# Optimization experiments

Hardware: AMD Instinct MI355X
Metric: run time of the kernel (lower is better)

Reference implementation:

```python
import math
import jax, jax.numpy as jnp
import numpy as np

B, S, D, H = 2, 1024, 4096, 32
HD = D // H  # 128


def _rope_freqs(seq_len, head_dim, theta=10000.0):
    inv = 1.0 / (theta ** (np.arange(0, head_dim, 2, dtype=np.float32) / head_dim))
    t = np.arange(seq_len, dtype=np.float32)
    ang = np.outer(t, inv)  # [S, HD/2]
    return jnp.asarray(np.cos(ang)), jnp.asarray(np.sin(ang))


def setup_inputs() -> dict:
    key = jax.random.key(0)
    ks = jax.random.split(key, 6)
    scale = 0.02
    x = jax.random.normal(ks[0], (B, S, D), dtype=jnp.float32)
    wq = jax.random.normal(ks[1], (D, D), dtype=jnp.float32) * scale
    wk = jax.random.normal(ks[2], (D, D), dtype=jnp.float32) * scale
    wv = jax.random.normal(ks[3], (D, D), dtype=jnp.float32) * scale
    wo = jax.random.normal(ks[4], (D, D), dtype=jnp.float32) * scale
    cache_k = jnp.zeros((B, S, H, HD), dtype=jnp.float32)
    cache_v = jnp.zeros((B, S, H, HD), dtype=jnp.float32)
    freqs_cos, freqs_sin = _rope_freqs(S, HD)
    return {"x": x, "wq": wq, "wk": wk, "wv": wv, "wo": wo,
            "cache_k": cache_k, "cache_v": cache_v,
            "freqs_cos": freqs_cos, "freqs_sin": freqs_sin, "start_pos": 0}


def _apply_rope(t, cos, sin):
    # t: [B, S, H, HD]; pairs (even, odd) along last dim form complex numbers
    t2 = t.reshape(*t.shape[:-1], HD // 2, 2)
    t0, t1 = t2[..., 0], t2[..., 1]
    c = cos[None, :, None, :]  # [1, S, 1, HD/2]
    s = sin[None, :, None, :]
    o0 = t0 * c - t1 * s
    o1 = t0 * s + t1 * c
    return jnp.stack([o0, o1], axis=-1).reshape(t.shape)


def reference(x, wq, wk, wv, wo, cache_k, cache_v, freqs_cos, freqs_sin, start_pos):
    b, s, d = x.shape
    q = (x @ wq.T).reshape(b, s, H, HD)
    k = (x @ wk.T).reshape(b, s, H, HD)  # n_kv_heads == n_heads (n_rep=1)
    v = (x @ wv.T).reshape(b, s, H, HD)
    q = _apply_rope(q, freqs_cos, freqs_sin)
    k = _apply_rope(k, freqs_cos, freqs_sin)
    # KV-cache write, then read the [0 : start_pos+s] window
    cache_k = cache_k.at[:b, start_pos:start_pos + s].set(k)
    cache_v = cache_v.at[:b, start_pos:start_pos + s].set(v)
    keys = cache_k[:b, :start_pos + s]    # [b, T, H, HD]
    values = cache_v[:b, :start_pos + s]
    scores = jnp.einsum("bqhd,bkhd->bhqk", q, keys) / math.sqrt(HD)
    attn = jax.nn.softmax(scores.astype(jnp.float32), axis=-1).astype(q.dtype)
    out = jnp.einsum("bhqk,bkhd->bqhd", attn, values).reshape(b, s, d)
    return out @ wo.T
```

## Files before the change

kernel.cpp:

```cpp
#include <hip/hip_runtime.h>

#define B_  2
#define S_  1024
#define D_  4096
#define H_  32
#define HD_ 128
#define T_  (B_*S_)

typedef short s16x8 __attribute__((ext_vector_type(8)));
typedef float f32x4 __attribute__((ext_vector_type(4)));
typedef unsigned short u16;

__device__ __forceinline__ u16 f2bf(float f) {
  unsigned int u = __float_as_uint(f);
  u += 0x7fffu + ((u >> 16) & 1u);
  return (u16)(u >> 16);
}
__device__ __forceinline__ float bf2f(u16 h) {
  return __uint_as_float(((unsigned int)h) << 16);
}
__device__ __forceinline__ void gload_lds16(const void* g, void* l) {
  __builtin_amdgcn_global_load_lds(
      (const __attribute__((address_space(1))) unsigned int*)g,
      (__attribute__((address_space(3))) unsigned int*)l, 16, 0, 0);
}
#define MFMA16(a, b, c) __builtin_amdgcn_mfma_f32_16x16x32_bf16((a), (b), (c), 0, 0, 0)

__global__ __launch_bounds__(256) void cvt_all(const float* __restrict__ x,
                                               const float* __restrict__ wq,
                                               const float* __restrict__ wk,
                                               const float* __restrict__ wv,
                                               const float* __restrict__ wo,
                                               u16* __restrict__ xb,
                                               u16* __restrict__ wb) {
  const int n8x = T_ * D_ / 8;
  const int n8w = D_ * D_ / 8;
  const int total = n8x + 4 * n8w;
  for (int i = blockIdx.x * 256 + threadIdx.x; i < total; i += gridDim.x * 256) {
    const float* src;
    u16* dst;
    int off;
    if (i < n8x) { src = x; dst = xb; off = i; }
    else {
      const int j = i - n8x;
      const int seg = j >> 21;
      off = j & (n8w - 1);
      src = (seg == 0) ? wq : (seg == 1) ? wk : (seg == 2) ? wv : wo;
      dst = wb + ((size_t)seg << 24);
    }
    const float4* p = (const float4*)src + (size_t)off * 2;
    float4 a = p[0], b = p[1];
    u16 us[8] = {f2bf(a.x), f2bf(a.y), f2bf(a.z), f2bf(a.w),
                 f2bf(b.x), f2bf(b.y), f2bf(b.z), f2bf(b.w)};
    *(uint4*)(dst + (size_t)off * 8) = *(uint4*)us;
  }
}

template <int NW>
__device__ __forceinline__ void stage_tile(const u16* __restrict__ g, int ldk,
                                           int row0, int k0, u16* lds,
                                           int wid, int lane) {
  const int rsub = lane >> 3;
  const int c16  = (lane & 7) ^ rsub;
#pragma unroll
  for (int l = 0; l < 16 / NW; ++l) {
    const int c = wid * (16 / NW) + l;
    gload_lds16(g + (size_t)(row0 + c * 8 + rsub) * ldk + k0 + c16 * 8,
                lds + c * 512);
  }
}

__global__ __launch_bounds__(256, 3) void gemm_qkv(const u16* __restrict__ A,
                                                   const u16* __restrict__ W,
                                                   u16* __restrict__ Oq,
                                                   u16* __restrict__ Ok,
                                                   u16* __restrict__ Ovt,
                                                   const float* __restrict__ cosb,
                                                   const float* __restrict__ sinb,
                                                   int MB, int NB, int K) {
  __shared__ __align__(16) u16 LA[128 * 64];
  __shared__ __align__(16) u16 LB[128 * 64];
  const int nwg = MB * NB;
  const int cpx = nwg >> 3;
  const int bid = blockIdx.x;
  const int swz = (bid & 7) * cpx + (bid >> 3);
  const int bm = swz / NB, bn = swz % NB;
  const int m0 = bm * 128, n0 = bn * 128;
  const int tid = threadIdx.x, wid = tid >> 6, lane = tid & 63;
  const int wr = wid >> 1, wc = wid & 1;
  const int fr = lane & 15, fq = lane >> 4;
  f32x4 acc[4][4] = {};

  for (int k0 = 0; k0 < K; k0 += 64) {
    stage_tile<4>(A, K, m0, k0, LA, wid, lane);
    stage_tile<4>(W, K, n0, k0, LB, wid, lane);
    __syncthreads();
    s16x8 bf[4][2];
#pragma unroll
    for (int ni = 0; ni < 4; ++ni)
#pragma unroll
      for (int kk = 0; kk < 2; ++kk) {
        const int rr = wc * 64 + ni * 16 + fr;
        const int s16 = (kk * 4 + fq) ^ (rr & 7);
        bf[ni][kk] = *(const s16x8*)&LB[rr * 64 + s16 * 8];
      }
#pragma unroll
    for (int mi = 0; mi < 4; ++mi) {
      const int r = wr * 64 + mi * 16 + fr;
      const s16x8 a0 = *(const s16x8*)&LA[r * 64 + ((0 + fq) ^ (r & 7)) * 8];
      const s16x8 a1 = *(const s16x8*)&LA[r * 64 + ((4 + fq) ^ (r & 7)) * 8];
#pragma unroll
      for (int ni = 0; ni < 4; ++ni)
        acc[mi][ni] = MFMA16(a0, bf[ni][0], acc[mi][ni]);
#pragma unroll
      for (int ni = 0; ni < 4; ++ni)
        acc[mi][ni] = MFMA16(a1, bf[ni][1], acc[mi][ni]);
    }
    __syncthreads();
  }

  if (n0 < 8192) {
    u16* Ob = (n0 < 4096) ? Oq : Ok;
    const int nc = n0 & 4095;
    const float sgn = (fr & 1) ? 1.f : -1.f;
#pragma unroll
    for (int mi = 0; mi < 4; ++mi)
#pragma unroll
      for (int ni = 0; ni < 4; ++ni) {
        const int col = nc + wc * 64 + ni * 16 + fr;
        const int i0 = (col & (HD_ - 1)) >> 1;
#pragma unroll
        for (int r = 0; r < 4; ++r) {
          const int row = m0 + wr * 64 + mi * 16 + fq * 4 + r;
          const int s = row & (S_ - 1);
          const float v  = acc[mi][ni][r];
          const float vo = __shfl_xor(v, 1);
          const float c  = cosb[s * (HD_ / 2) + i0];
          const float sn = sinb[s * (HD_ / 2) + i0];
          Ob[(size_t)row * 4096 + col] = f2bf(v * c + sgn * vo * sn);
        }
      }
  } else {
    const int nc = n0 - 8192;
#pragma unroll
    for (int mi = 0; mi < 4; ++mi)
#pragma unroll
      for (int ni = 0; ni < 4; ++ni) {
        const int col = nc + wc * 64 + ni * 16 + fr;
        const int h = col >> 7, d = col & (HD_ - 1);
        const int row0 = m0 + wr * 64 + mi * 16 + fq * 4;
        const int bb = row0 >> 10, s0 = row0 & (S_ - 1);
        ushort4 w;
        w.x = f2bf(acc[mi][ni][0]); w.y = f2bf(acc[mi][ni][1]);
        w.z = f2bf(acc[mi][ni][2]); w.w = f2bf(acc[mi][ni][3]);
        *(ushort4*)&Ovt[((size_t)(bb * H_ + h) * HD_ + d) * S_ + s0] = w;
      }
  }
}

__global__ __launch_bounds__(512, 2) void gemm2p_out(const u16* __restrict__ A,
                                                     const u16* __restrict__ W,
                                                     float* __restrict__ Of,
                                                     int MB, int NB, int K) {
  __shared__ __align__(16) u16 LA[2][128 * 64];
  __shared__ __align__(16) u16 LB[2][2][128 * 64];
  const int nwg = MB * NB;
  const int cpx = nwg >> 3;
  const int bid = blockIdx.x;
  const int swz = (bid & 7) * cpx + (bid >> 3);
  const int bm = swz / NB, bn = swz % NB;
  const int m0 = bm * 128, n0 = bn * 256;
  const int tid = threadIdx.x, wid = tid >> 6, lane = tid & 63;
  const int wr = wid >> 2, wc = wid & 3;
  const int fr = lane & 15, fq = lane >> 4;
  const int nkt = K >> 6;
  f32x4 acc[4][4] = {};

  auto STAGE = [&](int gidx) {
    if (gidx >= 3 * nkt) return;
    const int t = gidx / 3, part = gidx - 3 * t, slot = t & 1, k0 = t * 64;
    if (part < 2)
      stage_tile<8>(W, K, n0 + part * 128, k0, &LB[slot][part][0], wid, lane);
    else
      stage_tile<8>(A, K, m0, k0, &LA[slot][0], wid, lane);
  };

  for (int g = 0; g < 5; ++g) STAGE(g);
  asm volatile("s_waitcnt vmcnt(4)" ::: "memory");
  __builtin_amdgcn_s_barrier();

  for (int t = 0; t < nkt; ++t) {
    const int slot = t & 1;
    s16x8 af[2][2], bfr[4][2];
#pragma unroll
    for (int i = 0; i < 2; ++i)
#pragma unroll
      for (int kk = 0; kk < 2; ++kk) {
        const int r = wr * 64 + i * 16 + fr;
        const int s16 = (kk * 4 + fq) ^ (r & 7);
        af[i][kk] = *(const s16x8*)&LA[slot][r * 64 + s16 * 8];
      }
#pragma unroll
    for (int ni = 0; ni < 4; ++ni)
#pragma unroll
      for (int kk = 0; kk < 2; ++kk) {
        const int rr = (wc & 1) * 64 + ni * 16 + fr;
        const int s16 = (kk * 4 + fq) ^ (rr & 7);
        bfr[ni][kk] = *(const s16x8*)&LB[slot][wc >> 1][rr * 64 + s16 * 8];
      }
    STAGE(3 * t + 5);
    __builtin_amdgcn_s_barrier();
    __builtin_amdgcn_s_setprio(1);
#pragma unroll
    for (int kk = 0; kk < 2; ++kk)
#pragma unroll
      for (int i = 0; i < 2; ++i)
#pragma unroll
        for (int ni = 0; ni < 4; ++ni)
          acc[i][ni] = MFMA16(af[i][kk], bfr[ni][kk], acc[i][ni]);
    __builtin_amdgcn_s_setprio(0);
    __builtin_amdgcn_s_barrier();
#pragma unroll
    for (int i = 0; i < 2; ++i)
#pragma unroll
      for (int kk = 0; kk < 2; ++kk) {
        const int r = wr * 64 + (2 + i) * 16 + fr;
        const int s16 = (kk * 4 + fq) ^ (r & 7);
        af[i][kk] = *(const s16x8*)&LA[slot][r * 64 + s16 * 8];
      }
    STAGE(3 * t + 6);
    STAGE(3 * t + 7);
    if (t < nkt - 2) asm volatile("s_waitcnt vmcnt(4)" ::: "memory");
    else             asm volatile("s_waitcnt vmcnt(0)" ::: "memory");
    __builtin_amdgcn_s_barrier();
    __builtin_amdgcn_s_setprio(1);
#pragma unroll
    for (int kk = 0; kk < 2; ++kk)
#pragma unroll
      for (int i = 0; i < 2; ++i)
#pragma unroll
        for (int ni = 0; ni < 4; ++ni)
          acc[2 + i][ni] = MFMA16(af[i][kk], bfr[ni][kk], acc[2 + i][ni]);
    __builtin_amdgcn_s_setprio(0);
    __builtin_amdgcn_s_barrier();
  }

  const int Nn = NB * 256;
#pragma unroll
  for (int mi = 0; mi < 4; ++mi)
#pragma unroll
    for (int ni = 0; ni < 4; ++ni) {
      const int col = n0 + wc * 64 + ni * 16 + fr;
#pragma unroll
      for (int r = 0; r < 4; ++r) {
        const int row = m0 + wr * 64 + mi * 16 + fq * 4 + r;
        Of[(size_t)row * Nn + col] = acc[mi][ni][r];
      }
    }
}

__global__ __launch_bounds__(512) void flash_attn(const u16* __restrict__ qb,
                                                  const u16* __restrict__ kb,
                                                  const u16* __restrict__ vtb,
                                                  u16* __restrict__ ab) {
  __shared__ __align__(16) u16 Ks[64][136];
  __shared__ __align__(16) u16 Vs[128][72];
  __shared__ __align__(16) u16 Ps[8][16][72];
  const int qt = blockIdx.x, h = blockIdx.y, b = blockIdx.z;
  const int tid = threadIdx.x, wid = tid >> 6, lane = tid & 63;
  const int fr = lane & 15, fq = lane >> 4;
  const int q0 = qt * 128 + wid * 16;
  s16x8 qf[4];
  {
    size_t base = (size_t)(b * S_ + q0 + fr) * D_ + h * HD_;
#pragma unroll
    for (int kk = 0; kk < 4; ++kk) qf[kk] = *(const s16x8*)&qb[base + kk * 32 + fq * 8];
  }
  f32x4 oacc[8] = {};
  float m_i[4] = {-1e30f, -1e30f, -1e30f, -1e30f};
  float l_i[4] = {0.f, 0.f, 0.f, 0.f};
  const float sc = 0.08838834764831845f;

  for (int k0 = 0; k0 < S_; k0 += 64) {
    __syncthreads();
    for (int c = tid; c < 1024; c += 512) {
      int row = c >> 4, col = (c & 15) * 8;
      *(uint4*)&Ks[row][col] =
          *(const uint4*)&kb[(size_t)(b * S_ + k0 + row) * D_ + h * HD_ + col];
    }
    for (int c = tid; c < 1024; c += 512) {
      int row = c >> 3, col = (c & 7) * 8;
      *(uint4*)&Vs[row][col] =
          *(const uint4*)&vtb[(size_t)((b * H_ + h) * HD_ + row) * S_ + k0 + col];
    }
    __syncthreads();
    f32x4 sacc[4] = {};
    __builtin_amdgcn_s_setprio(1);
#pragma unroll
    for (int kk = 0; kk < 4; ++kk)
#pragma unroll
      for (int nb = 0; nb < 4; ++nb)
        sacc[nb] = MFMA16(qf[kk], *(const s16x8*)&Ks[nb * 16 + fr][kk * 32 + fq * 8],
                          sacc[nb]);
    __builtin_amdgcn_s_setprio(0);
#pragma unroll
    for (int r = 0; r < 4; ++r) {
      float s0 = sacc[0][r] * sc, s1 = sacc[1][r] * sc;
      float s2 = sacc[2][r] * sc, s3 = sacc[3][r] * sc;
      float mx = fmaxf(fmaxf(s0, s1), fmaxf(s2, s3));
#pragma unroll
      for (int o = 1; o < 16; o <<= 1) mx = fmaxf(mx, __shfl_xor(mx, o));
      float newm = fmaxf(m_i[r], mx);
      float fsc = __expf(m_i[r] - newm);
      m_i[r] = newm;
      float p0 = __expf(s0 - newm), p1 = __expf(s1 - newm);
      float p2 = __expf(s2 - newm), p3 = __expf(s3 - newm);
      float sum = p0 + p1 + p2 + p3;
#pragma unroll
      for (int o = 1; o < 16; o <<= 1) sum += __shfl_xor(sum, o);
      l_i[r] = l_i[r] * fsc + sum;
#pragma unroll
      for (int db = 0; db < 8; ++db) oacc[db][r] *= fsc;
      Ps[wid][fq * 4 + r][0 * 16 + fr] = f2bf(p0);
      Ps[wid][fq * 4 + r][1 * 16 + fr] = f2bf(p1);
      Ps[wid][fq * 4 + r][2 * 16 + fr] = f2bf(p2);
      Ps[wid][fq * 4 + r][3 * 16 + fr] = f2bf(p3);
    }
    s16x8 pf0 = *(const s16x8*)&Ps[wid][fr][fq * 8];
    s16x8 pf1 = *(const s16x8*)&Ps[wid][fr][32 + fq * 8];
    __builtin_amdgcn_s_setprio(1);
#pragma unroll
    for (int db = 0; db < 8; ++db)
      oacc[db] = MFMA16(pf0, *(const s16x8*)&Vs[db * 16 + fr][fq * 8], oacc[db]);
#pragma unroll
    for (int db = 0; db < 8; ++db)
      oacc[db] = MFMA16(pf1, *(const s16x8*)&Vs[db * 16 + fr][32 + fq * 8], oacc[db]);
    __builtin_amdgcn_s_setprio(0);
  }
#pragma unroll
  for (int r = 0; r < 4; ++r) {
    float inv = 1.0f / l_i[r];
    size_t rowbase = (size_t)(b * S_ + q0 + fq * 4 + r) * D_ + h * HD_;
#pragma unroll
    for (int db = 0; db < 8; ++db)
      ab[rowbase + db * 16 + fr] = f2bf(oacc[db][r] * inv);
  }
}

extern "C" void kernel_launch(void* const* d_in, const int* in_sizes, int n_in,
                              void* d_out, int out_size, void* d_ws, size_t ws_size,
                              hipStream_t stream) {
  const float* x    = (const float*)d_in[0];
  const float* wq   = (const float*)d_in[1];
  const float* wk   = (const float*)d_in[2];
  const float* wv   = (const float*)d_in[3];
  const float* wo   = (const float*)d_in[4];
  const float* fcos = (const float*)d_in[7];
  const float* fsin = (const float*)d_in[8];
  float* out = (float*)d_out;

  u16* xb  = (u16*)d_ws;
  u16* wqb = xb + (size_t)T_ * D_;
  u16* wob = wqb + 3 * (size_t)D_ * D_;
  u16* qb  = wob + (size_t)D_ * D_;
  u16* kb  = qb + (size_t)T_ * D_;
  u16* vtb = kb + (size_t)T_ * D_;
  u16* ab  = vtb + (size_t)T_ * D_;

  cvt_all<<<2048, 256, 0, stream>>>(x, wq, wk, wv, wo, xb, wqb);

  gemm_qkv<<<1536, 256, 0, stream>>>(xb, wqb, qb, kb, vtb, fcos, fsin, 16, 96, D_);

  flash_attn<<<dim3(S_ / 128, H_, B_), 512, 0, stream>>>(qb, kb, vtb, ab);

  gemm2p_out<<<256, 512, 0, stream>>>(ab, wob, out, 16, 16, D_);
}
```

Measured before the change: 500.0 us.

## Restructure QKV GEMM to 256x256 tiles with 8 warps and double-buffered async pipeline

Replaces the 128x128, 4-warp, single-buffered QKV projection GEMM with a 256x256, 8-warp kernel. Tile staging is split into four quarter-loads that are interleaved with the MFMA phases, and LDS is double-buffered with explicit vmcnt waits, barriers and setprio around the compute. Larger tiles raise data reuse and the pipeline hides global-to-LDS load latency. In exchange the kernel needs twice the accumulator registers and 128KB of LDS, and launches only 384 workgroups, which may leave the GPU underfilled.

Measured after the change: 530.7 us. +6.2%, slower.

```diff
diff --git a/kernel.cpp b/kernel.cpp
--- a/kernel.cpp
+++ b/kernel.cpp
@@ -70,53 +70,82 @@
   }
 }
 
-__global__ __launch_bounds__(256, 3) void gemm_qkv(const u16* __restrict__ A,
-                                                   const u16* __restrict__ W,
-                                                   u16* __restrict__ Oq,
-                                                   u16* __restrict__ Ok,
-                                                   u16* __restrict__ Ovt,
-                                                   const float* __restrict__ cosb,
-                                                   const float* __restrict__ sinb,
-                                                   int MB, int NB, int K) {
-  __shared__ __align__(16) u16 LA[128 * 64];
-  __shared__ __align__(16) u16 LB[128 * 64];
+__global__ __launch_bounds__(512, 2) void gemm_qkv8(const u16* __restrict__ A,
+                                                    const u16* __restrict__ W,
+                                                    u16* __restrict__ Oq,
+                                                    u16* __restrict__ Ok,
+                                                    u16* __restrict__ Ovt,
+                                                    const float* __restrict__ cosb,
+                                                    const float* __restrict__ sinb,
+                                                    int MB, int NB, int K) {
+  __shared__ __align__(16) u16 LA[2][2][128 * 64];
+  __shared__ __align__(16) u16 LB[2][2][128 * 64];
   const int nwg = MB * NB;
   const int cpx = nwg >> 3;
   const int bid = blockIdx.x;
   const int swz = (bid & 7) * cpx + (bid >> 3);
-  const int bm = swz / NB, bn = swz % NB;
-  const int m0 = bm * 128, n0 = bn * 128;
+  const int bm = swz % MB, bn = swz / MB;
+  const int m0 = bm * 256, n0 = bn * 256;
   const int tid = threadIdx.x, wid = tid >> 6, lane = tid & 63;
-  const int wr = wid >> 1, wc = wid & 1;
+  const int wr = wid >> 2, wc = wid & 3;
   const int fr = lane & 15, fq = lane >> 4;
-  f32x4 acc[4][4] = {};
-
-  for (int k0 = 0; k0 < K; k0 += 64) {
-    stage_tile<4>(A, K, m0, k0, LA, wid, lane);
-    stage_tile<4>(W, K, n0, k0, LB, wid, lane);
-    __syncthreads();
-    s16x8 bf[4][2];
-#pragma unroll
-    for (int ni = 0; ni < 4; ++ni)
-#pragma unroll
-      for (int kk = 0; kk < 2; ++kk) {
-        const int rr = wc * 64 + ni * 16 + fr;
-        const int s16 = (kk * 4 + fq) ^ (rr & 7);
-        bf[ni][kk] = *(const s16x8*)&LB[rr * 64 + s16 * 8];
-      }
-#pragma unroll
-    for (int mi = 0; mi < 4; ++mi) {
-      const int r = wr * 64 + mi * 16 + fr;
-      const s16x8 a0 = *(const s16x8*)&LA[r * 64 + ((0 + fq) ^ (r & 7)) * 8];
-      const s16x8 a1 = *(const s16x8*)&LA[r * 64 + ((4 + fq) ^ (r & 7)) * 8];
-#pragma unroll
-      for (int ni = 0; ni < 4; ++ni)
-        acc[mi][ni] = MFMA16(a0, bf[ni][0], acc[mi][ni]);
-#pragma unroll
-      for (int ni = 0; ni < 4; ++ni)
-        acc[mi][ni] = MFMA16(a1, bf[ni][1], acc[mi][ni]);
-    }
-    __syncthreads();
+  const int nkt = K >> 6;
+  f32x4 acc[8][4] = {};
+
+  auto STAGE = [&](int gidx) {
+    if (gidx >= 4 * nkt) return;
+    const int t = gidx >> 2, part = gidx & 3, slot = t & 1, k0 = t * 64;
+    if (part < 2)
+      stage_tile<8>(W, K, n0 + part * 128, k0, &LB[slot][part][0], wid, lane);
+    else
+      stage_tile<8>(A, K, m0 + (part - 2) * 128, k0, &LA[slot][part - 2][0], wid, lane);
+  };
+
+  for (int g = 0; g < 6; ++g) STAGE(g);
+  asm volatile("s_waitcnt vmcnt(4)" ::: "memory");
+  __builtin_amdgcn_s_barrier();
+
+  for (int t = 0; t < nkt; ++t) {
+    const int slot = t & 1;
+    s16x8 bfr[4][2];
+#pragma unroll
+    for (int q = 0; q < 4; ++q) {
+      s16x8 af[2][2];
+#pragma unroll
+      for (int i = 0; i < 2; ++i)
+#pragma unroll
+        for (int kk = 0; kk < 2; ++kk) {
+          const int r = (q * 2 + i) * 16 + fr;
+          const int s16 = (kk * 4 + fq) ^ (r & 7);
+          af[i][kk] = *(const s16x8*)&LA[slot][wr][r * 64 + s16 * 8];
+        }
+      if (q == 0) {
+#pragma unroll
+        for (int ni = 0; ni < 4; ++ni)
+#pragma unroll
+          for (int kk = 0; kk < 2; ++kk) {
+            const int rr = (wc & 1) * 64 + ni * 16 + fr;
+            const int s16 = (kk * 4 + fq) ^ (rr & 7);
+            bfr[ni][kk] = *(const s16x8*)&LB[slot][wc >> 1][rr * 64 + s16 * 8];
+          }
+      }
+      STAGE(4 * t + 6 + q);
+      if (q == 3) {
+        if (t < nkt - 2) asm volatile("s_waitcnt vmcnt(4)" ::: "memory");
+        else             asm volatile("s_waitcnt vmcnt(0)" ::: "memory");
+      }
+      __builtin_amdgcn_s_barrier();
+      __builtin_amdgcn_s_setprio(1);
+#pragma unroll
+      for (int kk = 0; kk < 2; ++kk)
+#pragma unroll
+        for (int i = 0; i < 2; ++i)
+#pragma unroll
+          for (int ni = 0; ni < 4; ++ni)
+            acc[q * 2 + i][ni] = MFMA16(af[i][kk], bfr[ni][kk], acc[q * 2 + i][ni]);
+      __builtin_amdgcn_s_setprio(0);
+      __builtin_amdgcn_s_barrier();
+    }
   }
 
   if (n0 < 8192) {
@@ -124,14 +153,14 @@
     const int nc = n0 & 4095;
     const float sgn = (fr & 1) ? 1.f : -1.f;
 #pragma unroll
-    for (int mi = 0; mi < 4; ++mi)
+    for (int mi = 0; mi < 8; ++mi)
 #pragma unroll
       for (int ni = 0; ni < 4; ++ni) {
         const int col = nc + wc * 64 + ni * 16 + fr;
         const int i0 = (col & (HD_ - 1)) >> 1;
 #pragma unroll
         for (int r = 0; r < 4; ++r) {
-          const int row = m0 + wr * 64 + mi * 16 + fq * 4 + r;
+          const int row = m0 + wr * 128 + mi * 16 + fq * 4 + r;
           const int s = row & (S_ - 1);
           const float v  = acc[mi][ni][r];
           const float vo = __shfl_xor(v, 1);
@@ -143,12 +172,12 @@
   } else {
     const int nc = n0 - 8192;
 #pragma unroll
-    for (int mi = 0; mi < 4; ++mi)
+    for (int mi = 0; mi < 8; ++mi)
 #pragma unroll
       for (int ni = 0; ni < 4; ++ni) {
         const int col = nc + wc * 64 + ni * 16 + fr;
         const int h = col >> 7, d = col & (HD_ - 1);
-        const int row0 = m0 + wr * 64 + mi * 16 + fq * 4;
+        const int row0 = m0 + wr * 128 + mi * 16 + fq * 4;
         const int bb = row0 >> 10, s0 = row0 & (S_ - 1);
         ushort4 w;
         w.x = f2bf(acc[mi][ni][0]); w.y = f2bf(acc[mi][ni][1]);
@@ -369,7 +398,7 @@
 
   cvt_all<<<2048, 256, 0, stream>>>(x, wq, wk, wv, wo, xb, wqb);
 
-  gemm_qkv<<<1536, 256, 0, stream>>>(xb, wqb, qb, kb, vtb, fcos, fsin, 16, 96, D_);
+  gemm_qkv8<<<384, 512, 0, stream>>>(xb, wqb, qb, kb, vtb, fcos, fsin, 8, 48, D_);
 
   flash_attn<<<dim3(S_ / 128, H_, B_), 512, 0, stream>>>(qb, kb, vtb, ab);
 
```

## Stage flash-attention K/V via direct-to-LDS loads with XOR swizzle; fold softmax scale into Q

Applied to the files above, without the earlier changes.

Flash attention now fills its K and V tiles with global_load_lds 16-byte transfers into XOR-swizzled LDS layouts instead of register round-trip uint4 copies, and the MFMA operand reads use the matching swizzle. This removes VGPR staging and padded layouts and is meant to avoid bank conflicts. The 1/sqrt(d) softmax scale is folded into the Q epilogue of the QKV GEMM, which drops per-score multiplies but rounds the scaled Q to bf16. The QKV GEMM block mapping is also changed to walk M fastest inside each swizzled group, which changes L2 reuse of the weight and activation tiles.

New measurement: 448.8 us. -10.2%, faster.

```diff
diff --git a/kernel.cpp b/kernel.cpp
--- a/kernel.cpp
+++ b/kernel.cpp
@@ -84,7 +84,7 @@
   const int cpx = nwg >> 3;
   const int bid = blockIdx.x;
   const int swz = (bid & 7) * cpx + (bid >> 3);
-  const int bm = swz / NB, bn = swz % NB;
+  const int bm = swz % MB, bn = swz / MB;
   const int m0 = bm * 128, n0 = bn * 128;
   const int tid = threadIdx.x, wid = tid >> 6, lane = tid & 63;
   const int wr = wid >> 1, wc = wid & 1;
@@ -121,6 +121,7 @@
 
   if (n0 < 8192) {
     u16* Ob = (n0 < 4096) ? Oq : Ok;
+    const float qsc = (n0 < 4096) ? 0.08838834764831845f : 1.0f;
     const int nc = n0 & 4095;
     const float sgn = (fr & 1) ? 1.f : -1.f;
 #pragma unroll
@@ -137,7 +138,7 @@
           const float vo = __shfl_xor(v, 1);
           const float c  = cosb[s * (HD_ / 2) + i0];
           const float sn = sinb[s * (HD_ / 2) + i0];
-          Ob[(size_t)row * 4096 + col] = f2bf(v * c + sgn * vo * sn);
+          Ob[(size_t)row * 4096 + col] = f2bf((v * c + sgn * vo * sn) * qsc);
         }
       }
   } else {
@@ -263,12 +264,14 @@
                                                   const u16* __restrict__ kb,
                                                   const u16* __restrict__ vtb,
                                                   u16* __restrict__ ab) {
-  __shared__ __align__(16) u16 Ks[64][136];
-  __shared__ __align__(16) u16 Vs[128][72];
+  __shared__ __align__(16) u16 Ks[128 * 64];
+  __shared__ __align__(16) u16 Vs[128 * 64];
   __shared__ __align__(16) u16 Ps[8][16][72];
   const int qt = blockIdx.x, h = blockIdx.y, b = blockIdx.z;
   const int tid = threadIdx.x, wid = tid >> 6, lane = tid & 63;
   const int fr = lane & 15, fq = lane >> 4;
+  const int rsub = lane >> 3;
+  const int c16  = (lane & 7) ^ rsub;
   const int q0 = qt * 128 + wid * 16;
   s16x8 qf[4];
   {
@@ -279,19 +282,19 @@
   f32x4 oacc[8] = {};
   float m_i[4] = {-1e30f, -1e30f, -1e30f, -1e30f};
   float l_i[4] = {0.f, 0.f, 0.f, 0.f};
-  const float sc = 0.08838834764831845f;
+  const u16* vsrc = vtb + (size_t)(b * H_ + h) * HD_ * S_;
 
   for (int k0 = 0; k0 < S_; k0 += 64) {
     __syncthreads();
-    for (int c = tid; c < 1024; c += 512) {
-      int row = c >> 4, col = (c & 15) * 8;
-      *(uint4*)&Ks[row][col] =
-          *(const uint4*)&kb[(size_t)(b * S_ + k0 + row) * D_ + h * HD_ + col];
-    }
-    for (int c = tid; c < 1024; c += 512) {
-      int row = c >> 3, col = (c & 7) * 8;
-      *(uint4*)&Vs[row][col] =
-          *(const uint4*)&vtb[(size_t)((b * H_ + h) * HD_ + row) * S_ + k0 + col];
+    {
+      const u16* ksrc = kb + (size_t)(b * S_ + k0) * D_ + h * HD_;
+#pragma unroll
+      for (int l = 0; l < 2; ++l) {
+        const int c = wid * 2 + l;
+        const int key = (c & 7) * 8 + rsub, half = c >> 3;
+        gload_lds16(ksrc + (size_t)key * D_ + half * 64 + c16 * 8, Ks + c * 512);
+      }
+      stage_tile<8>(vsrc, S_, 0, k0, Vs, wid, lane);
     }
     __syncthreads();
     f32x4 sacc[4] = {};
@@ -300,13 +303,15 @@
     for (int kk = 0; kk < 4; ++kk)
 #pragma unroll
       for (int nb = 0; nb < 4; ++nb)
-        sacc[nb] = MFMA16(qf[kk], *(const s16x8*)&Ks[nb * 16 + fr][kk * 32 + fq * 8],
-                          sacc[nb]);
+        sacc[nb] = MFMA16(qf[kk],
+            *(const s16x8*)&Ks[((kk >> 1) * 64 + nb * 16 + fr) * 64 +
+                               ((((kk & 1) * 4 + fq) ^ (fr & 7)) * 8)],
+            sacc[nb]);
     __builtin_amdgcn_s_setprio(0);
 #pragma unroll
     for (int r = 0; r < 4; ++r) {
-      float s0 = sacc[0][r] * sc, s1 = sacc[1][r] * sc;
-      float s2 = sacc[2][r] * sc, s3 = sacc[3][r] * sc;
+      float s0 = sacc[0][r], s1 = sacc[1][r];
+      float s2 = sacc[2][r], s3 = sacc[3][r];
       float mx = fmaxf(fmaxf(s0, s1), fmaxf(s2, s3));
 #pragma unroll
       for (int o = 1; o < 16; o <<= 1) mx = fmaxf(mx, __shfl_xor(mx, o));
@@ -331,10 +336,12 @@
     __builtin_amdgcn_s_setprio(1);
 #pragma unroll
     for (int db = 0; db < 8; ++db)
-      oacc[db] = MFMA16(pf0, *(const s16x8*)&Vs[db * 16 + fr][fq * 8], oacc[db]);
+      oacc[db] = MFMA16(pf0,
+          *(const s16x8*)&Vs[(db * 16 + fr) * 64 + ((fq ^ (fr & 7)) * 8)], oacc[db]);
 #pragma unroll
     for (int db = 0; db < 8; ++db)
-      oacc[db] = MFMA16(pf1, *(const s16x8*)&Vs[db * 16 + fr][32 + fq * 8], oacc[db]);
+      oacc[db] = MFMA16(pf1,
+          *(const s16x8*)&Vs[(db * 16 + fr) * 64 + (((4 + fq) ^ (fr & 7)) * 8)], oacc[db]);
     __builtin_amdgcn_s_setprio(0);
   }
 #pragma unroll
```
